# Performance work log

Measured on AMD Instinct MI355X. Metric: run time of the kernel, lower is better.

Reference implementation:

```python
import jax, jax.numpy as jnp
import numpy as np

N, S, T, E, H = 4, 2048, 2048, 512, 8
HD = E // H  # head_dim = 64


def setup_inputs() -> dict:
    key0 = jax.random.key(0)
    ks = jax.random.split(key0, 12)
    sc = 1.0 / np.sqrt(E)
    inp = {
        "query": jax.random.normal(ks[0], (N, S, E), jnp.float32),
        "key": jax.random.normal(ks[1], (N, T, E), jnp.float32),
        "value": jax.random.normal(ks[2], (N, T, E), jnp.float32),
        "attn_mask": jnp.tril(jnp.ones((S, T), jnp.int32)),  # causal: 0 => masked
        # nn.Linear weights (out, in) and biases, torch convention y = x @ W.T + b
        "Wq": jax.random.normal(ks[3], (E, E), jnp.float32) * sc,
        "bq": jax.random.normal(ks[4], (E,), jnp.float32) * sc,
        "Wk": jax.random.normal(ks[5], (E, E), jnp.float32) * sc,
        "bk": jax.random.normal(ks[6], (E,), jnp.float32) * sc,
        "Wv": jax.random.normal(ks[7], (E, E), jnp.float32) * sc,
        "bv": jax.random.normal(ks[8], (E,), jnp.float32) * sc,
        "Wp": jax.random.normal(ks[9], (E, E), jnp.float32) * sc,
        "bp": jax.random.normal(ks[10], (E,), jnp.float32) * sc,
    }
    return inp


def reference(query, key, value, attn_mask, Wq, bq, Wk, bk, Wv, bv, Wp, bp):
    # QKV projections, split heads: (N, H, L, HD)
    q = (query @ Wq.T + bq).reshape(N, S, H, HD).transpose(0, 2, 1, 3)
    k = (key @ Wk.T + bk).reshape(N, T, H, HD).transpose(0, 2, 1, 3)
    v = (value @ Wv.T + bv).reshape(N, T, H, HD).transpose(0, 2, 1, 3)
    # scaled scores (N, H, S, T) -- intentionally materialized like the original
    e = jnp.einsum("nhsd,nhtd->nhst", q, k) / jnp.sqrt(jnp.float32(HD))
    e = jnp.where(attn_mask == 0, -jnp.inf, e)
    a = jax.nn.softmax(e, axis=-1)
    # dropout is identity in eval mode (reference runs deterministic/eval)
    y = jnp.einsum("nhst,nhtd->nhsd", a, v)
    y = y.transpose(0, 2, 1, 3).reshape(N, S, E)
    return y @ Wp.T + bp
```

## Files before the change

### kernel.cpp

```cpp
#include <hip/hip_runtime.h>


#define DEV __device__ __forceinline__

typedef unsigned short u16;
typedef unsigned int u32;
typedef __bf16 bf16x8 __attribute__((ext_vector_type(8)));
typedef float f32x4 __attribute__((ext_vector_type(4)));

#define MFMA_BF16(A, B, C) __builtin_amdgcn_mfma_f32_16x16x32_bf16(A, B, C, 0, 0, 0)

DEV u16 f2bf(float f) {
  u32 u = __builtin_bit_cast(u32, f);
  u += 0x7fffu + ((u >> 16) & 1u);
  return (u16)(u >> 16);
}

DEV void cp16(void* l, const void* g) {
  __builtin_amdgcn_global_load_lds(
      (const __attribute__((address_space(1))) u32*)g,
      (__attribute__((address_space(3))) u32*)l, 16, 0, 0);
}

#define WAIT_VM(N) asm volatile("s_waitcnt vmcnt(" #N ")" ::: "memory")
#define WAIT_VMLG  asm volatile("s_waitcnt vmcnt(0) lgkmcnt(0)" ::: "memory")
#define WAIT_LG    asm volatile("s_waitcnt lgkmcnt(0)" ::: "memory")
#define BARRIER    asm volatile("s_barrier" ::: "memory")

__global__ __launch_bounds__(256) void cast_all(
    const float* __restrict__ q, const float* __restrict__ k, const float* __restrict__ v,
    const float* __restrict__ wq, const float* __restrict__ wk,
    const float* __restrict__ wv, const float* __restrict__ wp,
    u16* qo, u16* ko, u16* vo, u16* wqo, u16* wko, u16* wvo, u16* wpo) {
  int b = blockIdx.x;
  const float* s;
  u16* d;
  int i;
  if (b < 12288) {
    int t = b >> 12;
    s = (t == 0) ? q : (t == 1) ? k : v;
    d = (t == 0) ? qo : (t == 1) ? ko : vo;
    i = (b & 4095) * 256 + threadIdx.x;
  } else {
    int t = (b - 12288) >> 8;
    s = (t == 0) ? wq : (t == 1) ? wk : (t == 2) ? wv : wp;
    d = (t == 0) ? wqo : (t == 1) ? wko : (t == 2) ? wvo : wpo;
    i = ((b - 12288) & 255) * 256 + threadIdx.x;
  }
  float4 f = ((const float4*)s)[i];
  ushort4 o;
  o.x = f2bf(f.x); o.y = f2bf(f.y); o.z = f2bf(f.z); o.w = f2bf(f.w);
  ((ushort4*)d)[i] = o;
}

DEV void gemm_stage(const u16* __restrict__ A, const u16* __restrict__ W,
                    u16* As, u16* Bs, int m0, int n0, int kt, int tid) {
#pragma unroll
  for (int i = 0; i < 2; ++i) {
    int c = tid + 256 * i;
    int row = c >> 2, kc = (c & 3) * 8;
    cp16(&As[c * 8], A + (m0 + row) * 512 + kt + kc);
    cp16(&Bs[c * 8], W + (n0 + row) * 512 + kt + kc);
  }
}

DEV void gemm_loop(const u16* __restrict__ A, const u16* __restrict__ W,
                   u16* As, u16* Bs,
                   int m0, int n0, int tid, f32x4 acc[4][4]) {
  const int lane = tid & 63, wid = tid >> 6;
  const int wm = wid & 1, wn = wid >> 1;
  const int l15 = lane & 15, l4 = lane >> 4;
  gemm_stage(A, W, As, Bs, m0, n0, 0, tid);
  for (int it = 0; it < 16; ++it) {
    WAIT_VMLG;
    BARRIER;
    const u16* Ac = As + (it & 1) * 4096;
    const u16* Bc = Bs + (it & 1) * 4096;
    if (it < 15)
      gemm_stage(A, W, As + ((it + 1) & 1) * 4096, Bs + ((it + 1) & 1) * 4096,
                 m0, n0, (it + 1) * 32, tid);
    bf16x8 af[4], bfr[4];
#pragma unroll
    for (int f = 0; f < 4; ++f) {
      af[f]  = *(const bf16x8*)&Ac[(wm * 64 + f * 16 + l15) * 32 + l4 * 8];
      bfr[f] = *(const bf16x8*)&Bc[(wn * 64 + f * 16 + l15) * 32 + l4 * 8];
    }
    __builtin_amdgcn_s_setprio(1);
#pragma unroll
    for (int fm = 0; fm < 4; ++fm)
#pragma unroll
      for (int fn = 0; fn < 4; ++fn)
        acc[fm][fn] = MFMA_BF16(af[fm], bfr[fn], acc[fm][fn]);
    __builtin_amdgcn_s_setprio(0);
  }
}

__global__ __launch_bounds__(256) void gemm_qkv(
    const u16* __restrict__ qx, const u16* __restrict__ kx, const u16* __restrict__ vx,
    const u16* __restrict__ wq, const u16* __restrict__ wk, const u16* __restrict__ wv,
    const float* __restrict__ bq, const float* __restrict__ bk, const float* __restrict__ bv,
    u16* qp, u16* kp, u16* vp) {
  __shared__ u16 As[2 * 128 * 32];
  __shared__ u16 Bs[2 * 128 * 32];
  const int wsel = blockIdx.x >> 2;
  const u16* A = (wsel == 0) ? qx : (wsel == 1) ? kx : vx;
  const u16* W = (wsel == 0) ? wq : (wsel == 1) ? wk : wv;
  const float* bias = (wsel == 0) ? bq : (wsel == 1) ? bk : bv;
  u16* C = (wsel == 0) ? qp : (wsel == 1) ? kp : vp;
  const int n0 = (blockIdx.x & 3) * 128, m0 = blockIdx.y * 128;
  const int tid = threadIdx.x, lane = tid & 63, wid = tid >> 6;
  const int wm = wid & 1, wn = wid >> 1;
  const int l15 = lane & 15, l4 = lane >> 4;
  const float osc = (wsel == 0) ? 0.18033688f : 1.0f;

  f32x4 acc[4][4] = {};
  gemm_loop(A, W, As, Bs, m0, n0, tid, acc);

#pragma unroll
  for (int fn = 0; fn < 4; ++fn) {
    int col = n0 + wn * 64 + fn * 16 + l15;
    float bvv = bias[col];
#pragma unroll
    for (int fm = 0; fm < 4; ++fm) {
      int rowb = m0 + wm * 64 + fm * 16 + l4 * 4;
#pragma unroll
      for (int r = 0; r < 4; ++r)
        C[(rowb + r) * 512 + col] = f2bf((acc[fm][fn][r] + bvv) * osc);
    }
  }
}

__global__ __launch_bounds__(256) void gemm_out(const u16* __restrict__ A,
                                                const u16* __restrict__ W,
                                                const float* __restrict__ bias,
                                                float* __restrict__ C) {
  __shared__ u16 As[2 * 64 * 32];
  __shared__ u16 Bs[2 * 128 * 32];
  const int n0 = blockIdx.x * 128, m0 = blockIdx.y * 64;
  const int tid = threadIdx.x, lane = tid & 63, wid = tid >> 6;
  const int wm = wid & 1, wn = wid >> 1;
  const int l15 = lane & 15, l4 = lane >> 4;

  auto stage = [&](u16* Asb, u16* Bsb, int kt) {
    {
      int row = tid >> 2, kc = (tid & 3) * 8;
      cp16(&Asb[tid * 8], A + (m0 + row) * 512 + kt + kc);
    }
#pragma unroll
    for (int i = 0; i < 2; ++i) {
      int c = tid + 256 * i;
      int row = c >> 2, kc = (c & 3) * 8;
      cp16(&Bsb[c * 8], W + (n0 + row) * 512 + kt + kc);
    }
  };

  f32x4 acc[2][4] = {};
  stage(As, Bs, 0);
  for (int it = 0; it < 16; ++it) {
    WAIT_VMLG;
    BARRIER;
    const u16* Ac = As + (it & 1) * 2048;
    const u16* Bc = Bs + (it & 1) * 4096;
    if (it < 15)
      stage(As + ((it + 1) & 1) * 2048, Bs + ((it + 1) & 1) * 4096, (it + 1) * 32);
    bf16x8 af[2], bfr[4];
#pragma unroll
    for (int f = 0; f < 2; ++f)
      af[f] = *(const bf16x8*)&Ac[(wm * 32 + f * 16 + l15) * 32 + l4 * 8];
#pragma unroll
    for (int f = 0; f < 4; ++f)
      bfr[f] = *(const bf16x8*)&Bc[(wn * 64 + f * 16 + l15) * 32 + l4 * 8];
    __builtin_amdgcn_s_setprio(1);
#pragma unroll
    for (int fm = 0; fm < 2; ++fm)
#pragma unroll
      for (int fn = 0; fn < 4; ++fn)
        acc[fm][fn] = MFMA_BF16(af[fm], bfr[fn], acc[fm][fn]);
    __builtin_amdgcn_s_setprio(0);
  }

#pragma unroll
  for (int fn = 0; fn < 4; ++fn) {
    int col = n0 + wn * 64 + fn * 16 + l15;
    float bvv = bias[col];
#pragma unroll
    for (int fm = 0; fm < 2; ++fm) {
      int rowb = m0 + wm * 32 + fm * 16 + l4 * 4;
#pragma unroll
      for (int r = 0; r < 4; ++r)
        C[(rowb + r) * 512 + col] = acc[fm][fn][r] + bvv;
    }
  }
}

__global__ __launch_bounds__(256) void transpose_v(const u16* __restrict__ vp,
                                                   u16* __restrict__ vt) {
  __shared__ u16 L[64 * 72];
  const int bid = blockIdx.x;
  const int nh = bid & 31, tt = bid >> 5;
  const int n = nh >> 3, h = nh & 7;
  const u16* src = vp + (n * 2048 + tt * 64) * 512 + h * 64;
  const int tid = threadIdx.x;
#pragma unroll
  for (int i = 0; i < 2; ++i) {
    int c = tid + 256 * i;
    int row = c >> 3, dg = c & 7;
    uint4 x = *(const uint4*)(src + row * 512 + dg * 8);
    *(uint4*)&L[row * 72 + dg * 8] = x;
  }
  __syncthreads();
  u16* dst = vt + nh * 64 * 2048 + tt * 64;
#pragma unroll
  for (int i = 0; i < 2; ++i) {
    int c = tid + 256 * i;
    int d = c >> 3, tg = c & 7;
    u16 e[8];
#pragma unroll
    for (int j = 0; j < 8; ++j) {
      int tsrc = (tg & 4) * 8 + (tg & 3) * 4 + (j & 3) + (j >> 2) * 16;
      e[j] = L[tsrc * 72 + d];
    }
    uint4 o;
    o.x = (u32)e[0] | ((u32)e[1] << 16);
    o.y = (u32)e[2] | ((u32)e[3] << 16);
    o.z = (u32)e[4] | ((u32)e[5] << 16);
    o.w = (u32)e[6] | ((u32)e[7] << 16);
    *(uint4*)(dst + d * 2048 + tg * 8) = o;
  }
}

__global__ __launch_bounds__(256) void attn_kernel(const u16* __restrict__ Qg,
                                                   const u16* __restrict__ Kg,
                                                   const u16* __restrict__ Vt,
                                                   u16* __restrict__ Yg) {
  __shared__ u16 Qs[64 * 64];
  __shared__ u16 Ks[128 * 64];
  __shared__ u16 Vts[64 * 128];

  const int bid = blockIdx.x;
  const int nh = bid & 31;
  const int qt = 31 - (bid >> 5);
  const int n = nh >> 3, h = nh & 7;
  const int tid = threadIdx.x, lane = tid & 63, w = tid >> 6;
  const int l15 = lane & 15, l4 = lane >> 4;
  const int s0 = qt * 64;

  const u16* Qb = Qg + (n * 2048 + s0) * 512 + h * 64;
  const u16* Kb = Kg + n * 2048 * 512 + h * 64;
  const u16* Vb = Vt + nh * 64 * 2048;

#pragma unroll
  for (int i = 0; i < 2; ++i) {
    int c = tid + 256 * i;
    int row = c >> 3, dg = (c & 7) ^ (row & 7);
    cp16(&Qs[c * 8], Qb + row * 512 + dg * 8);
  }
#pragma unroll
  for (int i = 0; i < 4; ++i) {
    int c = tid + 256 * i;
    int t = c >> 3, dg = (c & 7) ^ (t & 7);
    cp16(&Ks[c * 8], Kb + t * 512 + dg * 8);
  }
#pragma unroll
  for (int i = 0; i < 4; ++i) {
    int c = tid + 256 * i;
    int d = c >> 4, x = c & 15;
    cp16(&Vts[c * 8], Vb + d * 2048 + ((x ^ (d & 15)) * 8));
  }
  WAIT_VM(8);
  BARRIER;
  const int qr = w * 16 + l15;
  bf16x8 qf0 = *(const bf16x8*)&Qs[qr * 64 + ((l4 ^ (qr & 7)) * 8)];
  bf16x8 qf1 = *(const bf16x8*)&Qs[qr * 64 + (((4 + l4) ^ (qr & 7)) * 8)];

  f32x4 accO[4] = {};
  float mrow = -1e30f, lrow = 0.f;
  const int sgl = s0 + w * 16 + l15;

  const int ntiles = (qt >> 1) + 1;
  for (int it = 0; it < ntiles; ++it) {
    const int t0 = it * 128;
    const bool more = (it + 1 < ntiles);

    WAIT_VM(4);
    BARRIER;

    f32x4 st[8];
    __builtin_amdgcn_s_setprio(1);
#pragma unroll
    for (int fn = 0; fn < 8; ++fn) {
      int tr = fn * 16 + l15;
      bf16x8 k0 = *(const bf16x8*)&Ks[tr * 64 + ((l4 ^ (tr & 7)) * 8)];
      bf16x8 k1 = *(const bf16x8*)&Ks[tr * 64 + (((4 + l4) ^ (tr & 7)) * 8)];
      f32x4 a = {};
      a = MFMA_BF16(k0, qf0, a);
      st[fn] = MFMA_BF16(k1, qf1, a);
    }
    __builtin_amdgcn_s_setprio(0);

    WAIT_LG;
    BARRIER;
    if (more) {
#pragma unroll
      for (int i = 0; i < 4; ++i) {
        int c = tid + 256 * i;
        int t = c >> 3, dg = (c & 7) ^ (t & 7);
        cp16(&Ks[c * 8], Kb + (t0 + 128 + t) * 512 + dg * 8);
      }
    }

    const bool diag = (t0 + 128 > s0);
    float rmax = -1e30f;
#pragma unroll
    for (int fn = 0; fn < 8; ++fn)
#pragma unroll
      for (int r = 0; r < 4; ++r) {
        float v = st[fn][r];
        if (diag) {
          int tg = t0 + fn * 16 + l4 * 4 + r;
          if (tg > sgl) v = -1e30f;
        }
        st[fn][r] = v;
        rmax = fmaxf(rmax, v);
      }
    rmax = fmaxf(rmax, __shfl_xor(rmax, 16));
    rmax = fmaxf(rmax, __shfl_xor(rmax, 32));
    if (__any(rmax > mrow + 10.f)) {
      float mnew = fmaxf(mrow, rmax);
      float alpha = __builtin_amdgcn_exp2f(mrow - mnew);
      mrow = mnew;
      lrow *= alpha;
      float aO[4];
#pragma unroll
      for (int r = 0; r < 4; ++r) aO[r] = __shfl(alpha, (lane & 48) | (l4 * 4 + r));
#pragma unroll
      for (int fd = 0; fd < 4; ++fd)
#pragma unroll
        for (int r = 0; r < 4; ++r) accO[fd][r] *= aO[r];
    }
    float rsum = 0.f;
#pragma unroll
    for (int fn = 0; fn < 8; ++fn)
#pragma unroll
      for (int r = 0; r < 4; ++r) {
        float p = __builtin_amdgcn_exp2f(st[fn][r] - mrow);
        st[fn][r] = p;
        rsum += p;
      }
    rsum += __shfl_xor(rsum, 16);
    rsum += __shfl_xor(rsum, 32);
    lrow += rsum;

    bf16x8 pa[4];
#pragma unroll
    for (int ks = 0; ks < 4; ++ks) {
      bf16x8 t;
      t[0] = (__bf16)st[2 * ks][0];     t[1] = (__bf16)st[2 * ks][1];
      t[2] = (__bf16)st[2 * ks][2];     t[3] = (__bf16)st[2 * ks][3];
      t[4] = (__bf16)st[2 * ks + 1][0]; t[5] = (__bf16)st[2 * ks + 1][1];
      t[6] = (__bf16)st[2 * ks + 1][2]; t[7] = (__bf16)st[2 * ks + 1][3];
      pa[ks] = t;
    }

    if (more) { WAIT_VM(4); }
    else      { WAIT_VM(0); }
    BARRIER;

    __builtin_amdgcn_s_setprio(1);
#pragma unroll
    for (int ks = 0; ks < 4; ++ks) {
#pragma unroll
      for (int fd = 0; fd < 4; ++fd) {
        int d = fd * 16 + l15;
        bf16x8 bv = *(const bf16x8*)&Vts[d * 128 + (((ks * 4 + l4) ^ l15) * 8)];
        accO[fd] = MFMA_BF16(pa[ks], bv, accO[fd]);
      }
    }
    __builtin_amdgcn_s_setprio(0);

    WAIT_LG;
    BARRIER;
    if (more) {
#pragma unroll
      for (int i = 0; i < 4; ++i) {
        int c = tid + 256 * i;
        int d = c >> 4, x = c & 15;
        cp16(&Vts[c * 8], Vb + d * 2048 + (t0 + 128) + ((x ^ (d & 15)) * 8));
      }
    }
  }

  float lO[4];
#pragma unroll
  for (int r = 0; r < 4; ++r) lO[r] = __shfl(lrow, (lane & 48) | (l4 * 4 + r));
#pragma unroll
  for (int fd = 0; fd < 4; ++fd)
#pragma unroll
    for (int r = 0; r < 4; ++r) {
      int row = s0 + w * 16 + l4 * 4 + r;
      int col = h * 64 + fd * 16 + l15;
      Yg[(n * 2048 + row) * 512 + col] = f2bf(accO[fd][r] / lO[r]);
    }
}

extern "C" void kernel_launch(void* const* d_in, const int* in_sizes, int n_in,
                              void* d_out, int out_size, void* d_ws, size_t ws_size,
                              hipStream_t stream) {
  (void)in_sizes; (void)n_in; (void)out_size; (void)ws_size;
  const float* query = (const float*)d_in[0];
  const float* key_  = (const float*)d_in[1];
  const float* value = (const float*)d_in[2];
  const float* Wq = (const float*)d_in[4];
  const float* bq = (const float*)d_in[5];
  const float* Wk = (const float*)d_in[6];
  const float* bk = (const float*)d_in[7];
  const float* Wv = (const float*)d_in[8];
  const float* bv = (const float*)d_in[9];
  const float* Wp = (const float*)d_in[10];
  const float* bp = (const float*)d_in[11];

  char* ws = (char*)d_ws;
  u16* qx  = (u16*)(ws);
  u16* kx  = (u16*)(ws + 8388608);
  u16* vx  = (u16*)(ws + 16777216);
  u16* wqx = (u16*)(ws + 25165824);
  u16* wkx = (u16*)(ws + 25690112);
  u16* wvx = (u16*)(ws + 26214400);
  u16* wpx = (u16*)(ws + 26738688);
  u16* qp  = (u16*)(ws + 27262976);
  u16* kp  = (u16*)(ws + 35651584);
  u16* vp  = (u16*)(ws + 44040192);
  u16* y   = qx;
  u16* vt  = kx;

  cast_all<<<13312, 256, 0, stream>>>(query, key_, value, Wq, Wk, Wv, Wp,
                                      qx, kx, vx, wqx, wkx, wvx, wpx);
  gemm_qkv<<<dim3(12, 64), 256, 0, stream>>>(qx, kx, vx, wqx, wkx, wvx,
                                             bq, bk, bv, qp, kp, vp);
  transpose_v<<<1024, 256, 0, stream>>>(vp, vt);
  attn_kernel<<<1024, 256, 0, stream>>>(qp, kp, vt, y);
  gemm_out<<<dim3(4, 128), 256, 0, stream>>>(y, wpx, bp, (float*)d_out);
}
```

Before: 195.2 us.

## Pair complementary causal query tiles per block for balanced attention work

Each attention block now handles two query tiles, a high one and a low one (qt and 31-qt), running a fixed 17 KV-tile loop. In the middle of that loop it writes out the first tile's output and resets the softmax state. The grid halves to 512 blocks so every block does equal work, removing the tail imbalance of causal masking. The row max and row sum reductions are also rewritten as vectorized trees. The costs are more Q shared memory and less parallelism, since there are fewer blocks to hide latency.

```diff
diff --git a/kernel.cpp b/kernel.cpp
--- a/kernel.cpp
+++ b/kernel.cpp
@@ -233,27 +233,37 @@
                                                    const u16* __restrict__ Kg,
                                                    const u16* __restrict__ Vt,
                                                    u16* __restrict__ Yg) {
-  __shared__ u16 Qs[64 * 64];
+  __shared__ u16 Qs[2 * 64 * 64];
   __shared__ u16 Ks[128 * 64];
   __shared__ u16 Vts[64 * 128];
 
   const int bid = blockIdx.x;
   const int nh = bid & 31;
-  const int qt = 31 - (bid >> 5);
+  const int pairIdx = bid >> 5;
   const int n = nh >> 3, h = nh & 7;
   const int tid = threadIdx.x, lane = tid & 63, w = tid >> 6;
   const int l15 = lane & 15, l4 = lane >> 4;
-  const int s0 = qt * 64;
-
-  const u16* Qb = Qg + (n * 2048 + s0) * 512 + h * 64;
+
+  const int qtH = 31 - pairIdx, qtL = pairIdx;
+  const bool swp = pairIdx & 1;
+  const int qtFirst = swp ? qtL : qtH;
+  const int qtSecond = swp ? qtH : qtL;
+  const int ntFirst = (qtFirst >> 1) + 1;
+
+  int s0 = qtFirst * 64;
+  const int s0Second = qtSecond * 64;
+
+  const u16* QbF = Qg + (n * 2048 + s0) * 512 + h * 64;
+  const u16* QbS = Qg + (n * 2048 + s0Second) * 512 + h * 64;
   const u16* Kb = Kg + n * 2048 * 512 + h * 64;
   const u16* Vb = Vt + nh * 64 * 2048;
 
 #pragma unroll
-  for (int i = 0; i < 2; ++i) {
-    int c = tid + 256 * i;
-    int row = c >> 3, dg = (c & 7) ^ (row & 7);
-    cp16(&Qs[c * 8], Qb + row * 512 + dg * 8);
+  for (int i = 0; i < 4; ++i) {
+    int c = tid + 256 * i;
+    int which = c >> 9, row = (c >> 3) & 63, dg = (c & 7) ^ (row & 7);
+    const u16* qb = which ? QbS : QbF;
+    cp16(&Qs[c * 8], qb + row * 512 + dg * 8);
   }
 #pragma unroll
   for (int i = 0; i < 4; ++i) {
@@ -275,15 +285,42 @@
 
   f32x4 accO[4] = {};
   float mrow = -1e30f, lrow = 0.f;
-  const int sgl = s0 + w * 16 + l15;
-
-  const int ntiles = (qt >> 1) + 1;
-  for (int it = 0; it < ntiles; ++it) {
-    const int t0 = it * 128;
-    const bool more = (it + 1 < ntiles);
+  int sgl = s0 + w * 16 + l15;
+
+  auto writeO = [&]() {
+    float lO[4];
+#pragma unroll
+    for (int r = 0; r < 4; ++r) lO[r] = __shfl(lrow, (lane & 48) | (l4 * 4 + r));
+#pragma unroll
+    for (int fd = 0; fd < 4; ++fd)
+#pragma unroll
+      for (int r = 0; r < 4; ++r) {
+        int row = s0 + w * 16 + l4 * 4 + r;
+        int col = h * 64 + fd * 16 + l15;
+        Yg[(n * 2048 + row) * 512 + col] = f2bf(accO[fd][r] / lO[r]);
+      }
+  };
+
+  for (int it = 0; it < 17; ++it) {
+    const int lit = (it < ntFirst) ? it : it - ntFirst;
+    const int t0 = lit * 128;
+    const bool more = (it + 1 < 17);
+    const int nit = it + 1;
+    const int t0n = ((nit < ntFirst) ? nit : nit - ntFirst) * 128;
 
     WAIT_VM(4);
     BARRIER;
+
+    if (it == ntFirst) {
+      writeO();
+#pragma unroll
+      for (int fd = 0; fd < 4; ++fd) accO[fd] = f32x4{};
+      mrow = -1e30f; lrow = 0.f;
+      s0 = s0Second;
+      sgl = s0 + w * 16 + l15;
+      qf0 = *(const bf16x8*)&Qs[4096 + qr * 64 + ((l4 ^ (qr & 7)) * 8)];
+      qf1 = *(const bf16x8*)&Qs[4096 + qr * 64 + (((4 + l4) ^ (qr & 7)) * 8)];
+    }
 
     f32x4 st[8];
     __builtin_amdgcn_s_setprio(1);
@@ -305,24 +342,27 @@
       for (int i = 0; i < 4; ++i) {
         int c = tid + 256 * i;
         int t = c >> 3, dg = (c & 7) ^ (t & 7);
-        cp16(&Ks[c * 8], Kb + (t0 + 128 + t) * 512 + dg * 8);
+        cp16(&Ks[c * 8], Kb + (t0n + t) * 512 + dg * 8);
       }
     }
 
     const bool diag = (t0 + 128 > s0);
-    float rmax = -1e30f;
-#pragma unroll
-    for (int fn = 0; fn < 8; ++fn)
-#pragma unroll
-      for (int r = 0; r < 4; ++r) {
-        float v = st[fn][r];
-        if (diag) {
+    if (diag) {
+#pragma unroll
+      for (int fn = 0; fn < 8; ++fn)
+#pragma unroll
+        for (int r = 0; r < 4; ++r) {
           int tg = t0 + fn * 16 + l4 * 4 + r;
-          if (tg > sgl) v = -1e30f;
+          if (tg > sgl) st[fn][r] = -1e30f;
         }
-        st[fn][r] = v;
-        rmax = fmaxf(rmax, v);
-      }
+    }
+    f32x4 ma = __builtin_elementwise_max(st[0], st[1]);
+    f32x4 mb = __builtin_elementwise_max(st[2], st[3]);
+    f32x4 mc = __builtin_elementwise_max(st[4], st[5]);
+    f32x4 md = __builtin_elementwise_max(st[6], st[7]);
+    f32x4 m4 = __builtin_elementwise_max(__builtin_elementwise_max(ma, mb),
+                                         __builtin_elementwise_max(mc, md));
+    float rmax = fmaxf(fmaxf(m4[0], m4[1]), fmaxf(m4[2], m4[3]));
     rmax = fmaxf(rmax, __shfl_xor(rmax, 16));
     rmax = fmaxf(rmax, __shfl_xor(rmax, 32));
     if (__any(rmax > mrow + 10.f)) {
@@ -338,15 +378,16 @@
 #pragma unroll
         for (int r = 0; r < 4; ++r) accO[fd][r] *= aO[r];
     }
-    float rsum = 0.f;
 #pragma unroll
     for (int fn = 0; fn < 8; ++fn)
 #pragma unroll
-      for (int r = 0; r < 4; ++r) {
-        float p = __builtin_amdgcn_exp2f(st[fn][r] - mrow);
-        st[fn][r] = p;
-        rsum += p;
-      }
+      for (int r = 0; r < 4; ++r)
+        st[fn][r] = __builtin_amdgcn_exp2f(st[fn][r] - mrow);
+    f32x4 s4 = st[0] + st[1];
+    s4 += st[2] + st[3];
+    s4 += st[4] + st[5];
+    s4 += st[6] + st[7];
+    float rsum = (s4[0] + s4[1]) + (s4[2] + s4[3]);
     rsum += __shfl_xor(rsum, 16);
     rsum += __shfl_xor(rsum, 32);
     lrow += rsum;
@@ -385,22 +426,12 @@
       for (int i = 0; i < 4; ++i) {
         int c = tid + 256 * i;
         int d = c >> 4, x = c & 15;
-        cp16(&Vts[c * 8], Vb + d * 2048 + (t0 + 128) + ((x ^ (d & 15)) * 8));
+        cp16(&Vts[c * 8], Vb + d * 2048 + t0n + ((x ^ (d & 15)) * 8));
       }
     }
   }
 
-  float lO[4];
-#pragma unroll
-  for (int r = 0; r < 4; ++r) lO[r] = __shfl(lrow, (lane & 48) | (l4 * 4 + r));
-#pragma unroll
-  for (int fd = 0; fd < 4; ++fd)
-#pragma unroll
-    for (int r = 0; r < 4; ++r) {
-      int row = s0 + w * 16 + l4 * 4 + r;
-      int col = h * 64 + fd * 16 + l15;
-      Yg[(n * 2048 + row) * 512 + col] = f2bf(accO[fd][r] / lO[r]);
-    }
+  writeO();
 }
 
 extern "C" void kernel_launch(void* const* d_in, const int* in_sizes, int n_in,
@@ -438,6 +469,6 @@
   gemm_qkv<<<dim3(12, 64), 256, 0, stream>>>(qx, kx, vx, wqx, wkx, wvx,
                                              bq, bk, bv, qp, kp, vp);
   transpose_v<<<1024, 256, 0, stream>>>(vp, vt);
-  attn_kernel<<<1024, 256, 0, stream>>>(qp, kp, vt, y);
+  attn_kernel<<<512, 256, 0, stream>>>(qp, kp, vt, y);
   gemm_out<<<dim3(4, 128), 256, 0, stream>>>(y, wpx, bp, (float*)d_out);
 }
```

Result: no change. 198.3 us (+1.6%).

## Fuse V transpose into QKV GEMM epilogue and rebalance attention block order

Applied to the files above, without the earlier changes.

The V projection epilogue now writes directly into the transposed, permuted Vt layout the attention kernel expects, which removes the separate transpose_v kernel and its extra global round trip. The attention kernel also gets a new block-to-query-tile mapping through a fixed permutation table that pairs long and short causal tiles so work is spread more evenly across CUs. K/V load addresses are precomputed and advanced incrementally, and the row max and row sum reductions are vectorised into tree reductions. The V epilogue now does scattered 8-byte stores instead of row-contiguous stores, which may be less coalesced.

```diff
diff --git a/kernel.cpp b/kernel.cpp
--- a/kernel.cpp
+++ b/kernel.cpp
@@ -99,33 +99,56 @@
     const u16* __restrict__ qx, const u16* __restrict__ kx, const u16* __restrict__ vx,
     const u16* __restrict__ wq, const u16* __restrict__ wk, const u16* __restrict__ wv,
     const float* __restrict__ bq, const float* __restrict__ bk, const float* __restrict__ bv,
-    u16* qp, u16* kp, u16* vp) {
+    u16* qp, u16* kp, u16* vtO) {
   __shared__ u16 As[2 * 128 * 32];
   __shared__ u16 Bs[2 * 128 * 32];
   const int wsel = blockIdx.x >> 2;
   const u16* A = (wsel == 0) ? qx : (wsel == 1) ? kx : vx;
   const u16* W = (wsel == 0) ? wq : (wsel == 1) ? wk : wv;
   const float* bias = (wsel == 0) ? bq : (wsel == 1) ? bk : bv;
-  u16* C = (wsel == 0) ? qp : (wsel == 1) ? kp : vp;
   const int n0 = (blockIdx.x & 3) * 128, m0 = blockIdx.y * 128;
   const int tid = threadIdx.x, lane = tid & 63, wid = tid >> 6;
   const int wm = wid & 1, wn = wid >> 1;
   const int l15 = lane & 15, l4 = lane >> 4;
-  const float osc = (wsel == 0) ? 0.18033688f : 1.0f;
 
   f32x4 acc[4][4] = {};
   gemm_loop(A, W, As, Bs, m0, n0, tid, acc);
 
-#pragma unroll
-  for (int fn = 0; fn < 4; ++fn) {
-    int col = n0 + wn * 64 + fn * 16 + l15;
-    float bvv = bias[col];
-#pragma unroll
-    for (int fm = 0; fm < 4; ++fm) {
-      int rowb = m0 + wm * 64 + fm * 16 + l4 * 4;
-#pragma unroll
-      for (int r = 0; r < 4; ++r)
-        C[(rowb + r) * 512 + col] = f2bf((acc[fm][fn][r] + bvv) * osc);
+  if (wsel == 2) {
+#pragma unroll
+    for (int fn = 0; fn < 4; ++fn) {
+      int col = n0 + wn * 64 + fn * 16 + l15;
+      float bvv = bias[col];
+      int h = col >> 6, d = col & 63;
+#pragma unroll
+      for (int fm = 0; fm < 4; ++fm) {
+        int rowb = m0 + wm * 64 + fm * 16 + l4 * 4;
+        int nb = rowb >> 11, t = rowb & 2047;
+        int t64 = t & 63, tt = t >> 6;
+        int tg = ((t64 >> 5) << 2) | ((t64 >> 2) & 3);
+        int j0 = ((t64 >> 4) & 1) << 2;
+        ushort4 o;
+        o.x = f2bf(acc[fm][fn][0] + bvv);
+        o.y = f2bf(acc[fm][fn][1] + bvv);
+        o.z = f2bf(acc[fm][fn][2] + bvv);
+        o.w = f2bf(acc[fm][fn][3] + bvv);
+        *(ushort4*)&vtO[((nb * 8 + h) * 64 + d) * 2048 + tt * 64 + tg * 8 + j0] = o;
+      }
+    }
+  } else {
+    u16* C = (wsel == 0) ? qp : kp;
+    const float osc = (wsel == 0) ? 0.18033688f : 1.0f;
+#pragma unroll
+    for (int fn = 0; fn < 4; ++fn) {
+      int col = n0 + wn * 64 + fn * 16 + l15;
+      float bvv = bias[col];
+#pragma unroll
+      for (int fm = 0; fm < 4; ++fm) {
+        int rowb = m0 + wm * 64 + fm * 16 + l4 * 4;
+#pragma unroll
+        for (int r = 0; r < 4; ++r)
+          C[(rowb + r) * 512 + col] = f2bf((acc[fm][fn][r] + bvv) * osc);
+      }
     }
   }
 }
@@ -193,42 +216,6 @@
   }
 }
 
-__global__ __launch_bounds__(256) void transpose_v(const u16* __restrict__ vp,
-                                                   u16* __restrict__ vt) {
-  __shared__ u16 L[64 * 72];
-  const int bid = blockIdx.x;
-  const int nh = bid & 31, tt = bid >> 5;
-  const int n = nh >> 3, h = nh & 7;
-  const u16* src = vp + (n * 2048 + tt * 64) * 512 + h * 64;
-  const int tid = threadIdx.x;
-#pragma unroll
-  for (int i = 0; i < 2; ++i) {
-    int c = tid + 256 * i;
-    int row = c >> 3, dg = c & 7;
-    uint4 x = *(const uint4*)(src + row * 512 + dg * 8);
-    *(uint4*)&L[row * 72 + dg * 8] = x;
-  }
-  __syncthreads();
-  u16* dst = vt + nh * 64 * 2048 + tt * 64;
-#pragma unroll
-  for (int i = 0; i < 2; ++i) {
-    int c = tid + 256 * i;
-    int d = c >> 3, tg = c & 7;
-    u16 e[8];
-#pragma unroll
-    for (int j = 0; j < 8; ++j) {
-      int tsrc = (tg & 4) * 8 + (tg & 3) * 4 + (j & 3) + (j >> 2) * 16;
-      e[j] = L[tsrc * 72 + d];
-    }
-    uint4 o;
-    o.x = (u32)e[0] | ((u32)e[1] << 16);
-    o.y = (u32)e[2] | ((u32)e[3] << 16);
-    o.z = (u32)e[4] | ((u32)e[5] << 16);
-    o.w = (u32)e[6] | ((u32)e[7] << 16);
-    *(uint4*)(dst + d * 2048 + tg * 8) = o;
-  }
-}
-
 __global__ __launch_bounds__(256) void attn_kernel(const u16* __restrict__ Qg,
                                                    const u16* __restrict__ Kg,
                                                    const u16* __restrict__ Vt,
@@ -237,9 +224,13 @@
   __shared__ u16 Ks[128 * 64];
   __shared__ u16 Vts[64 * 128];
 
+  static const int Nt[16] = {16, 1, 12, 5,  9, 8, 13, 4,  2, 15, 6, 11,  7, 10, 3, 14};
+
   const int bid = blockIdx.x;
-  const int nh = bid & 31;
-  const int qt = 31 - (bid >> 5);
+  const int nh = (bid & 7) | (((bid >> 5) & 3) << 3);
+  const int u = (bid >> 3) & 3, s = (bid >> 7) & 1, r4 = bid >> 8;
+  const int nt = Nt[r4 * 4 + u];
+  const int qt = 2 * (nt - 1) + s;
   const int n = nh >> 3, h = nh & 7;
   const int tid = threadIdx.x, lane = tid & 63, w = tid >> 6;
   const int l15 = lane & 15, l4 = lane >> 4;
@@ -249,6 +240,20 @@
   const u16* Kb = Kg + n * 2048 * 512 + h * 64;
   const u16* Vb = Vt + nh * 64 * 2048;
 
+  const u16* kSrc[4];
+  const u16* vSrc[4];
+  int kDst[4], vDst[4];
+#pragma unroll
+  for (int i = 0; i < 4; ++i) {
+    int c = tid + 256 * i;
+    int t = c >> 3, dg = (c & 7) ^ (t & 7);
+    kSrc[i] = Kb + t * 512 + dg * 8;
+    kDst[i] = c * 8;
+    int d = c >> 4, x = c & 15;
+    vSrc[i] = Vb + d * 2048 + ((x ^ (d & 15)) * 8);
+    vDst[i] = c * 8;
+  }
+
 #pragma unroll
   for (int i = 0; i < 2; ++i) {
     int c = tid + 256 * i;
@@ -256,17 +261,10 @@
     cp16(&Qs[c * 8], Qb + row * 512 + dg * 8);
   }
 #pragma unroll
-  for (int i = 0; i < 4; ++i) {
-    int c = tid + 256 * i;
-    int t = c >> 3, dg = (c & 7) ^ (t & 7);
-    cp16(&Ks[c * 8], Kb + t * 512 + dg * 8);
-  }
-#pragma unroll
-  for (int i = 0; i < 4; ++i) {
-    int c = tid + 256 * i;
-    int d = c >> 4, x = c & 15;
-    cp16(&Vts[c * 8], Vb + d * 2048 + ((x ^ (d & 15)) * 8));
-  }
+  for (int i = 0; i < 4; ++i) { cp16(&Ks[kDst[i]], kSrc[i]); kSrc[i] += 128 * 512; }
+#pragma unroll
+  for (int i = 0; i < 4; ++i) { cp16(&Vts[vDst[i]], vSrc[i]); vSrc[i] += 128; }
+
   WAIT_VM(8);
   BARRIER;
   const int qr = w * 16 + l15;
@@ -277,10 +275,9 @@
   float mrow = -1e30f, lrow = 0.f;
   const int sgl = s0 + w * 16 + l15;
 
-  const int ntiles = (qt >> 1) + 1;
-  for (int it = 0; it < ntiles; ++it) {
+  for (int it = 0; it < nt; ++it) {
     const int t0 = it * 128;
-    const bool more = (it + 1 < ntiles);
+    const bool more = (it + 1 < nt);
 
     WAIT_VM(4);
     BARRIER;
@@ -302,27 +299,26 @@
     BARRIER;
     if (more) {
 #pragma unroll
-      for (int i = 0; i < 4; ++i) {
-        int c = tid + 256 * i;
-        int t = c >> 3, dg = (c & 7) ^ (t & 7);
-        cp16(&Ks[c * 8], Kb + (t0 + 128 + t) * 512 + dg * 8);
-      }
+      for (int i = 0; i < 4; ++i) { cp16(&Ks[kDst[i]], kSrc[i]); kSrc[i] += 128 * 512; }
     }
 
     const bool diag = (t0 + 128 > s0);
-    float rmax = -1e30f;
-#pragma unroll
-    for (int fn = 0; fn < 8; ++fn)
-#pragma unroll
-      for (int r = 0; r < 4; ++r) {
-        float v = st[fn][r];
-        if (diag) {
+    if (diag) {
+#pragma unroll
+      for (int fn = 0; fn < 8; ++fn)
+#pragma unroll
+        for (int r = 0; r < 4; ++r) {
           int tg = t0 + fn * 16 + l4 * 4 + r;
-          if (tg > sgl) v = -1e30f;
+          if (tg > sgl) st[fn][r] = -1e30f;
         }
-        st[fn][r] = v;
-        rmax = fmaxf(rmax, v);
-      }
+    }
+    f32x4 ma = __builtin_elementwise_max(st[0], st[1]);
+    f32x4 mb = __builtin_elementwise_max(st[2], st[3]);
+    f32x4 mc = __builtin_elementwise_max(st[4], st[5]);
+    f32x4 md = __builtin_elementwise_max(st[6], st[7]);
+    f32x4 m4 = __builtin_elementwise_max(__builtin_elementwise_max(ma, mb),
+                                         __builtin_elementwise_max(mc, md));
+    float rmax = fmaxf(fmaxf(m4[0], m4[1]), fmaxf(m4[2], m4[3]));
     rmax = fmaxf(rmax, __shfl_xor(rmax, 16));
     rmax = fmaxf(rmax, __shfl_xor(rmax, 32));
     if (__any(rmax > mrow + 10.f)) {
@@ -338,15 +334,16 @@
 #pragma unroll
         for (int r = 0; r < 4; ++r) accO[fd][r] *= aO[r];
     }
-    float rsum = 0.f;
 #pragma unroll
     for (int fn = 0; fn < 8; ++fn)
 #pragma unroll
-      for (int r = 0; r < 4; ++r) {
-        float p = __builtin_amdgcn_exp2f(st[fn][r] - mrow);
-        st[fn][r] = p;
-        rsum += p;
-      }
+      for (int r = 0; r < 4; ++r)
+        st[fn][r] = __builtin_amdgcn_exp2f(st[fn][r] - mrow);
+    f32x4 s4 = st[0] + st[1];
+    s4 += st[2] + st[3];
+    s4 += st[4] + st[5];
+    s4 += st[6] + st[7];
+    float rsum = (s4[0] + s4[1]) + (s4[2] + s4[3]);
     rsum += __shfl_xor(rsum, 16);
     rsum += __shfl_xor(rsum, 32);
     lrow += rsum;
@@ -382,11 +379,7 @@
     BARRIER;
     if (more) {
 #pragma unroll
-      for (int i = 0; i < 4; ++i) {
-        int c = tid + 256 * i;
-        int d = c >> 4, x = c & 15;
-        cp16(&Vts[c * 8], Vb + d * 2048 + (t0 + 128) + ((x ^ (d & 15)) * 8));
-      }
+      for (int i = 0; i < 4; ++i) { cp16(&Vts[vDst[i]], vSrc[i]); vSrc[i] += 128; }
     }
   }
 
@@ -429,15 +422,13 @@
   u16* wpx = (u16*)(ws + 26738688);
   u16* qp  = (u16*)(ws + 27262976);
   u16* kp  = (u16*)(ws + 35651584);
-  u16* vp  = (u16*)(ws + 44040192);
+  u16* vt  = (u16*)(ws + 44040192);
   u16* y   = qx;
-  u16* vt  = kx;
 
   cast_all<<<13312, 256, 0, stream>>>(query, key_, value, Wq, Wk, Wv, Wp,
                                       qx, kx, vx, wqx, wkx, wvx, wpx);
   gemm_qkv<<<dim3(12, 64), 256, 0, stream>>>(qx, kx, vx, wqx, wkx, wvx,
-                                             bq, bk, bv, qp, kp, vp);
-  transpose_v<<<1024, 256, 0, stream>>>(vp, vt);
+                                             bq, bk, bv, qp, kp, vt);
   attn_kernel<<<1024, 256, 0, stream>>>(qp, kp, vt, y);
   gemm_out<<<dim3(4, 128), 256, 0, stream>>>(y, wpx, bp, (float*)d_out);
 }
```

Result: slower. 205.5 us (+5.2%).
